# Kernel optimization log

Hardware: AMD Instinct MI355X
Metric: run time of the kernel (lower is better)

Reference implementation:

```python
import jax, jax.numpy as jnp
import numpy as np

B, R, L = 1, 256, 384
IN_DIM, PAIR_DIM, N_HEADS = 128, 128, 8
HEAD_DIM = IN_DIM // N_HEADS
FF_MULT = 4


def layer_norm(x, g, b, eps=1e-5):
    mu = jnp.mean(x, axis=-1, keepdims=True)
    var = jnp.mean((x - mu) ** 2, axis=-1, keepdims=True)
    return (x - mu) * jax.lax.rsqrt(var + eps) * g + b


def setup_inputs() -> dict:
    key = jax.random.key(0)
    ks = jax.random.split(key, 12)
    s = 0.02
    return {
        "x": jax.random.normal(ks[0], (B, L, L, PAIR_DIM), jnp.float32),
        "m": jax.random.normal(ks[1], (B, R, L, IN_DIM), jnp.float32),
        "ln1_g": jnp.ones((PAIR_DIM,), jnp.float32),
        "ln1_b": jnp.zeros((PAIR_DIM,), jnp.float32),
        "ln2_g": jnp.ones((IN_DIM,), jnp.float32),
        "ln2_b": jnp.zeros((IN_DIM,), jnp.float32),
        "ln3_g": jnp.ones((IN_DIM,), jnp.float32),
        "ln3_b": jnp.zeros((IN_DIM,), jnp.float32),
        "w1": jax.random.normal(ks[2], (PAIR_DIM, N_HEADS), jnp.float32) * s,
        "b1": jnp.zeros((N_HEADS,), jnp.float32),
        "w2": jax.random.normal(ks[3], (IN_DIM, HEAD_DIM), jnp.float32) * s,
        "b2": jnp.zeros((HEAD_DIM,), jnp.float32),
        "ffw1": jax.random.normal(ks[4], (IN_DIM, IN_DIM * FF_MULT), jnp.float32) * s,
        "ffb1": jnp.zeros((IN_DIM * FF_MULT,), jnp.float32),
        "ffw2": jax.random.normal(ks[5], (IN_DIM * FF_MULT, IN_DIM), jnp.float32) * s,
        "ffb2": jnp.zeros((IN_DIM,), jnp.float32),
    }


def reference(x, m, ln1_g, ln1_b, ln2_g, ln2_b, ln3_g, ln3_b,
              w1, b1, w2, b2, ffw1, ffb1, ffw2, ffb2):
    # symmetrize pair features: [b, i, j, d]
    pair = (x + jnp.swapaxes(x, 1, 2)) * 0.5
    pair = layer_norm(pair, ln1_g, ln1_b)
    # attention logits per head, softmax over j (axis=-2): [b, i, j, h]
    attn = jax.nn.softmax(pair @ w1 + b1, axis=-2)
    # values: [b, r, j, d_head]
    values = layer_norm(m, ln2_g, ln2_b) @ w2 + b2
    # [b,i,j,h] x [b,r,j,d] -> [b,r,i,h,d]
    attn_out = jnp.einsum('bijh,brjd->brihd', attn, values)
    attn_out = attn_out.reshape(*attn_out.shape[:3], -1)  # [b,r,i,h*d]
    out = m + attn_out
    residue = layer_norm(out, ln3_g, ln3_b)
    ff = jax.nn.relu(residue @ ffw1 + ffb1) @ ffw2 + ffb2  # dropout off (eval)
    return out + ff
```

## Files before the change

### kernel.cpp

```cpp
#include <hip/hip_runtime.h>

typedef __attribute__((ext_vector_type(8))) short bf16x8;
typedef __attribute__((ext_vector_type(4))) float f32x4;

constexpr int L  = 384;
constexpr int R  = 256;
constexpr int D  = 128;
constexpr int NH = 8;
constexpr int HD = 16;
constexpr int FF = 512;

#define MFMA16(a, b, c) __builtin_amdgcn_mfma_f32_16x16x32_bf16((a), (b), (c), 0, 0, 0)

__device__ inline unsigned short f2bf(float f) {
    unsigned u = __builtin_bit_cast(unsigned, f);
    u += 0x7fffu + ((u >> 16) & 1u);
    return (unsigned short)(u >> 16);
}
__device__ inline float bf2f(unsigned short h) {
    unsigned u = ((unsigned)h) << 16;
    return __builtin_bit_cast(float, u);
}

__device__ inline int tri_row(int q) {
    int i = (int)((769.0f - sqrtf((float)(591361 - 8 * q))) * 0.5f);
    while ((i + 1) * (769 - (i + 1)) / 2 <= q) ++i;
    while (i * (769 - i) / 2 > q) --i;
    return i;
}

__global__ void k_prep(const float* __restrict__ w1,
                       const float* __restrict__ w2,
                       const float* __restrict__ ffw1,
                       const float* __restrict__ ffw2,
                       const float* __restrict__ g3,
                       const float* __restrict__ b3,
                       const float* __restrict__ ffb1,
                       unsigned short* __restrict__ w1p,
                       unsigned short* __restrict__ w2p,
                       unsigned short* __restrict__ w1gF,
                       unsigned short* __restrict__ w2tF,
                       float2* __restrict__ c1c2) {
    const int idx = blockIdx.x * 256 + threadIdx.x;
    {
        const int fi = idx >> 9, rem = idx & 511, l = rem >> 3, e = rem & 7;
        const int lr2 = l & 15, lg2 = l >> 4;
        const int n = fi >> 2, ks = fi & 3;
        const int ch = n * 16 + lr2, k = ks * 32 + lg2 * 8 + e;
        w1gF[idx] = f2bf(g3[k] * ffw1[(size_t)k * FF + ch]);
    }
    {
        const int fi = idx >> 9, rem = idx & 511, l = rem >> 3, e = rem & 7;
        const int lr2 = l & 15, lg2 = l >> 4;
        const int n = fi >> 4, Ks = fi & 15;
        const int ch = n * 16 + lr2, k = Ks * 32 + lg2 * 8 + e;
        w2tF[idx] = f2bf(ffw2[(size_t)k * D + ch]);
    }
    if (idx < 16 * D) {
        const int n = idx >> 7, k = idx & 127;
        w1p[idx] = (n < NH) ? f2bf(w1[(size_t)k * NH + n]) : (unsigned short)0;
        w2p[idx] = f2bf(w2[(size_t)k * HD + n]);
    }
    if (blockIdx.x < 2) {
        const int n = blockIdx.x * 256 + threadIdx.x;
        float c1 = 0.f, c2 = 0.f;
        for (int k = 0; k < D; ++k) {
            const float w = ffw1[(size_t)k * FF + n];
            c1 += g3[k] * w;
            c2 += b3[k] * w;
        }
        c1c2[n] = make_float2(c1, c2 + ffb1[n]);
    }
}

__global__ void k_pair_logits(const float* __restrict__ x,
                              const float* __restrict__ g,
                              const float* __restrict__ bt,
                              const unsigned short* __restrict__ w1p,
                              const float* __restrict__ b1,
                              float* __restrict__ logits) {
    __shared__ unsigned short nrm[64][136];
    __shared__ int ij[64];
    const int tid = threadIdx.x;
    const int q0 = blockIdx.x * 64;

    {
        const int pr = tid >> 2, part = tid & 3;
        const int q = q0 + pr;
        const int i = tri_row(q);
        const int j = i + (q - i * (769 - i) / 2);
        if (part == 0) ij[pr] = (i << 16) | j;
        const float* xa = x + ((size_t)i * L + j) * D + part * 32;
        const float* xb = x + ((size_t)j * L + i) * D + part * 32;
        float v[32];
        float s = 0.f, sq = 0.f;
        #pragma unroll
        for (int q8 = 0; q8 < 8; ++q8) {
            const float4 a = ((const float4*)xa)[q8];
            const float4 b = ((const float4*)xb)[q8];
            const float t0 = 0.5f * (a.x + b.x), t1 = 0.5f * (a.y + b.y);
            const float t2 = 0.5f * (a.z + b.z), t3 = 0.5f * (a.w + b.w);
            v[q8*4+0] = t0; v[q8*4+1] = t1; v[q8*4+2] = t2; v[q8*4+3] = t3;
            s  += t0 + t1 + t2 + t3;
            sq += t0*t0 + t1*t1 + t2*t2 + t3*t3;
        }
        s  += __shfl_xor(s, 1);  s  += __shfl_xor(s, 2);
        sq += __shfl_xor(sq, 1); sq += __shfl_xor(sq, 2);
        const float mean = s * (1.0f / D);
        const float rstd = rsqrtf(sq * (1.0f / D) - mean * mean + 1e-5f);
        #pragma unroll
        for (int q8 = 0; q8 < 8; ++q8) {
            const int c = part * 32 + q8 * 4;
            ushort4 pk;
            pk.x = f2bf((v[q8*4+0] - mean) * rstd * g[c+0] + bt[c+0]);
            pk.y = f2bf((v[q8*4+1] - mean) * rstd * g[c+1] + bt[c+1]);
            pk.z = f2bf((v[q8*4+2] - mean) * rstd * g[c+2] + bt[c+2]);
            pk.w = f2bf((v[q8*4+3] - mean) * rstd * g[c+3] + bt[c+3]);
            *(ushort4*)(&nrm[pr][c]) = pk;
        }
    }
    __syncthreads();

    {
        const int wv = tid >> 6, lane = tid & 63;
        const int lr = lane & 15, lg = lane >> 4;
        f32x4 acc = {0.f, 0.f, 0.f, 0.f};
        #pragma unroll
        for (int ks = 0; ks < 4; ++ks) {
            bf16x8 a = *(const bf16x8*)(&nrm[wv * 16 + lr][ks * 32 + lg * 8]);
            bf16x8 b = *(const bf16x8*)(w1p + (size_t)lr * D + ks * 32 + lg * 8);
            acc = MFMA16(a, b, acc);
        }
        if (lr < NH) {
            #pragma unroll
            for (int r = 0; r < 4; ++r) {
                const int pl = wv * 16 + lg * 4 + r;
                const int pij = ij[pl];
                const int pi = pij >> 16, pj = pij & 0xffff;
                const float val = acc[r] + b1[lr];
                logits[((size_t)pi * L + pj) * NH + lr] = val;
                logits[((size_t)pj * L + pi) * NH + lr] = val;
            }
        }
    }
}

__global__ void k_softmax(const float* __restrict__ logits,
                          unsigned short* __restrict__ attnT) {
    const int wave = blockIdx.x * 4 + (threadIdx.x >> 6);
    const int lane = threadIdx.x & 63;
    const int i = wave >> 3, h = wave & 7;

    float v[6];
    float mx = -1e30f;
    #pragma unroll
    for (int t = 0; t < 6; ++t) {
        const int j = lane + t * 64;
        v[t] = logits[((size_t)i * L + j) * NH + h];
        mx = fmaxf(mx, v[t]);
    }
    #pragma unroll
    for (int msk = 32; msk; msk >>= 1) mx = fmaxf(mx, __shfl_xor(mx, msk));

    float s = 0.0f;
    #pragma unroll
    for (int t = 0; t < 6; ++t) { v[t] = __expf(v[t] - mx); s += v[t]; }
    #pragma unroll
    for (int msk = 32; msk; msk >>= 1) s += __shfl_xor(s, msk);
    const float inv = 1.0f / s;

    #pragma unroll
    for (int t = 0; t < 6; ++t) {
        const int j = lane + t * 64;
        attnT[((size_t)h * L + i) * L + j] = f2bf(v[t] * inv);
    }
}

__global__ void k_values(const float* __restrict__ min_,
                         const float* __restrict__ g,
                         const float* __restrict__ bt,
                         const unsigned short* __restrict__ w2p,
                         const float* __restrict__ b2,
                         unsigned short* __restrict__ VtT) {
    __shared__ unsigned short nrm[128][136];
    const int tid = threadIdx.x;
    const int r  = blockIdx.x;
    const int j0 = blockIdx.y * 128;

    #pragma unroll
    for (int half = 0; half < 2; ++half) {
        const int row  = half * 64 + (tid >> 2);
        const int part = tid & 3;
        const float* src = min_ + ((size_t)r * L + j0 + row) * D + part * 32;
        float v[32];
        float s = 0.f, sq = 0.f;
        #pragma unroll
        for (int q = 0; q < 8; ++q) {
            const float4 a = ((const float4*)src)[q];
            v[q*4+0] = a.x; v[q*4+1] = a.y; v[q*4+2] = a.z; v[q*4+3] = a.w;
            s  += a.x + a.y + a.z + a.w;
            sq += a.x*a.x + a.y*a.y + a.z*a.z + a.w*a.w;
        }
        s  += __shfl_xor(s, 1);  s  += __shfl_xor(s, 2);
        sq += __shfl_xor(sq, 1); sq += __shfl_xor(sq, 2);
        const float mean = s * (1.0f / D);
        const float rstd = rsqrtf(sq * (1.0f / D) - mean * mean + 1e-5f);
        #pragma unroll
        for (int q = 0; q < 8; ++q) {
            const int c = part * 32 + q * 4;
            ushort4 pk;
            pk.x = f2bf((v[q*4+0] - mean) * rstd * g[c+0] + bt[c+0]);
            pk.y = f2bf((v[q*4+1] - mean) * rstd * g[c+1] + bt[c+1]);
            pk.z = f2bf((v[q*4+2] - mean) * rstd * g[c+2] + bt[c+2]);
            pk.w = f2bf((v[q*4+3] - mean) * rstd * g[c+3] + bt[c+3]);
            *(ushort4*)(&nrm[row][c]) = pk;
        }
    }
    __syncthreads();

    {
        const int wv = tid >> 6, lane = tid & 63;
        const int lr = lane & 15, lg = lane >> 4;
        f32x4 acc[2];
        acc[0] = (f32x4){0.f, 0.f, 0.f, 0.f};
        acc[1] = (f32x4){0.f, 0.f, 0.f, 0.f};
        #pragma unroll
        for (int ks = 0; ks < 4; ++ks) {
            bf16x8 b = *(const bf16x8*)(w2p + (size_t)lr * D + ks * 32 + lg * 8);
            #pragma unroll
            for (int mt = 0; mt < 2; ++mt) {
                bf16x8 a = *(const bf16x8*)(&nrm[wv * 32 + mt * 16 + lr][ks * 32 + lg * 8]);
                acc[mt] = MFMA16(a, b, acc[mt]);
            }
        }
        const float bb = b2[lr];
        #pragma unroll
        for (int mt = 0; mt < 2; ++mt) {
            ushort4 pk;
            pk.x = f2bf(acc[mt][0] + bb);
            pk.y = f2bf(acc[mt][1] + bb);
            pk.z = f2bf(acc[mt][2] + bb);
            pk.w = f2bf(acc[mt][3] + bb);
            *(ushort4*)(VtT + (size_t)(r * HD + lr) * L + j0 + wv * 32 + mt * 16 + lg * 4) = pk;
        }
    }
}

__global__ void k_attn_out(const unsigned short* __restrict__ attnT,
                           const unsigned short* __restrict__ VtT,
                           const float* __restrict__ min_,
                           unsigned short* __restrict__ outb) {
    const int h  = blockIdx.z;
    const int i0 = blockIdx.x * 128;
    const int n0 = blockIdx.y * 128;
    const int tid = threadIdx.x, wv = tid >> 6, lane = tid & 63;
    const int lr = lane & 15, lg = lane >> 4;
    const int wio = (wv >> 1) * 64, wno = (wv & 1) * 64;
    const unsigned short* Abase = attnT + (size_t)h * L * L;

    f32x4 acc[4][4];
    #pragma unroll
    for (int a = 0; a < 4; ++a)
        #pragma unroll
        for (int b = 0; b < 4; ++b) acc[a][b] = (f32x4){0.f, 0.f, 0.f, 0.f};

    bf16x8 af[4], bf[4], afn[4], bfn[4];
    #pragma unroll
    for (int mt = 0; mt < 4; ++mt)
        af[mt] = *(const bf16x8*)(Abase + (size_t)(i0 + wio + mt * 16 + lr) * L + lg * 8);
    #pragma unroll
    for (int nt = 0; nt < 4; ++nt)
        bf[nt] = *(const bf16x8*)(VtT + (size_t)(n0 + wno + nt * 16 + lr) * L + lg * 8);

    for (int ks = 0; ks < 12; ++ks) {
        if (ks < 11) {
            const int ko = (ks + 1) * 32 + lg * 8;
            #pragma unroll
            for (int mt = 0; mt < 4; ++mt)
                afn[mt] = *(const bf16x8*)(Abase + (size_t)(i0 + wio + mt * 16 + lr) * L + ko);
            #pragma unroll
            for (int nt = 0; nt < 4; ++nt)
                bfn[nt] = *(const bf16x8*)(VtT + (size_t)(n0 + wno + nt * 16 + lr) * L + ko);
        }
        #pragma unroll
        for (int mt = 0; mt < 4; ++mt)
            #pragma unroll
            for (int nt = 0; nt < 4; ++nt)
                acc[mt][nt] = MFMA16(af[mt], bf[nt], acc[mt][nt]);
        #pragma unroll
        for (int q = 0; q < 4; ++q) { af[q] = afn[q]; bf[q] = bfn[q]; }
    }

    #pragma unroll
    for (int mt = 0; mt < 4; ++mt) {
        #pragma unroll
        for (int nt = 0; nt < 4; ++nt) {
            const int nbase = n0 + wno + nt * 16;
            const int rrow  = nbase >> 4;
            #pragma unroll
            for (int r = 0; r < 4; ++r) {
                const int i = i0 + wio + mt * 16 + lg * 4 + r;
                const size_t gidx = ((size_t)rrow * L + i) * D + h * HD + lr;
                outb[gidx] = f2bf(min_[gidx] + acc[mt][nt][r]);
            }
        }
    }
}

__global__ __launch_bounds__(512, 4) void k_ffn(
                      const unsigned short* __restrict__ outb,
                      const unsigned short* __restrict__ w1gF,
                      const float2* __restrict__ c1c2,
                      const unsigned short* __restrict__ w2tF,
                      const float* __restrict__ ffb2,
                      float* __restrict__ out) {
    __shared__ unsigned short At[64 * 128];
    __shared__ unsigned short hid[2][64 * 128];
    __shared__ float2 stats[64];
    const int tid = threadIdx.x;
    const size_t row0 = (size_t)blockIdx.x * 64;

    const int wv = tid >> 6, lane = tid & 63;
    const int lr = lane & 15, lg = lane >> 4;
    const int wm = wv >> 2, wn = wv & 3;

    bf16x8 w1f[8], w2f[8];
    #pragma unroll
    for (int ks = 0; ks < 4; ++ks)
        #pragma unroll
        for (int nt = 0; nt < 2; ++nt) {
            const int fi = (0 * 8 + wn * 2 + nt) * 4 + ks;
            w1f[ks * 2 + nt] = *(const bf16x8*)((const char*)w1gF + fi * 1024 + lane * 16);
        }

    {
        const int rr = tid >> 3, part = tid & 7;
        const unsigned short* src = outb + (row0 + rr) * D + part * 16;
        const uint4 v0 = *(const uint4*)(src);
        const uint4 v1 = *(const uint4*)(src + 8);
        float s = 0.f, sq = 0.f;
        const unsigned w[8] = {v0.x, v0.y, v0.z, v0.w, v1.x, v1.y, v1.z, v1.w};
        #pragma unroll
        for (int e = 0; e < 8; ++e) {
            const float lo = __builtin_bit_cast(float, w[e] << 16);
            const float hi = __builtin_bit_cast(float, w[e] & 0xffff0000u);
            s  += lo + hi;
            sq += lo * lo + hi * hi;
        }
        s  += __shfl_xor(s, 1);  s  += __shfl_xor(s, 2);  s  += __shfl_xor(s, 4);
        sq += __shfl_xor(sq, 1); sq += __shfl_xor(sq, 2); sq += __shfl_xor(sq, 4);
        if (part == 0) {
            const float mean = s * (1.0f / D);
            const float rstd = rsqrtf(sq * (1.0f / D) - mean * mean + 1e-5f);
            stats[rr] = make_float2(rstd, mean * rstd);
        }
        const int xr = (rr & 7) << 4;
        char* rowp = (char*)(At + rr * 128);
        const int cb = part * 32;
        *(uint4*)(rowp + ((cb     ) ^ xr)) = v0;
        *(uint4*)(rowp + ((cb + 16) ^ xr)) = v1;
    }

    #pragma unroll
    for (int ks = 0; ks < 4; ++ks)
        #pragma unroll
        for (int nt = 0; nt < 2; ++nt) {
            const int fi = (wn * 2 + nt) * 16 + 0 * 4 + ks;
            w2f[ks * 2 + nt] = *(const bf16x8*)((const char*)w2tF + fi * 1024 + lane * 16);
        }

    __syncthreads();

    f32x4 acc2[2][2];
    #pragma unroll
    for (int m = 0; m < 2; ++m)
        #pragma unroll
        for (int n = 0; n < 2; ++n) acc2[m][n] = (f32x4){0.f, 0.f, 0.f, 0.f};

    #pragma unroll
    for (int kc = 0; kc < 4; ++kc) {
        const int p = kc & 1;

        {
            f32x4 acc1[2][2];
            #pragma unroll
            for (int m = 0; m < 2; ++m)
                #pragma unroll
                for (int n = 0; n < 2; ++n) acc1[m][n] = (f32x4){0.f, 0.f, 0.f, 0.f};

            #pragma unroll
            for (int ks = 0; ks < 4; ++ks) {
                bf16x8 af[2];
                #pragma unroll
                for (int mt = 0; mt < 2; ++mt) {
                    const int row = wm * 32 + mt * 16 + lr;
                    af[mt] = *(const bf16x8*)((char*)(At + row * 128) +
                              ((ks * 64 + lg * 16) ^ ((row & 7) << 4)));
                }
                #pragma unroll
                for (int mt = 0; mt < 2; ++mt)
                    #pragma unroll
                    for (int nt = 0; nt < 2; ++nt)
                        acc1[mt][nt] = MFMA16(af[mt], w1f[ks * 2 + nt], acc1[mt][nt]);
            }

            #pragma unroll
            for (int nt = 0; nt < 2; ++nt) {
                const int chl = wn * 32 + nt * 16 + lr;
                const float2 cc = c1c2[kc * 128 + chl];
                #pragma unroll
                for (int mt = 0; mt < 2; ++mt) {
                    #pragma unroll
                    for (int r = 0; r < 4; ++r) {
                        const int row = wm * 32 + mt * 16 + lg * 4 + r;
                        const float2 st = stats[row];
                        const float pre = st.x * acc1[mt][nt][r] - st.y * cc.x + cc.y;
                        *(unsigned short*)((char*)(hid[p] + row * 128) +
                            ((chl * 2) ^ ((row & 7) << 4))) = f2bf(fmaxf(pre, 0.f));
                    }
                }
            }
        }
        __syncthreads();

        if (kc < 3) {
            #pragma unroll
            for (int ks = 0; ks < 4; ++ks)
                #pragma unroll
                for (int nt = 0; nt < 2; ++nt) {
                    const int fi = ((kc + 1) * 8 + wn * 2 + nt) * 4 + ks;
                    w1f[ks * 2 + nt] = *(const bf16x8*)((const char*)w1gF + fi * 1024 + lane * 16);
                }
        }

        {
            #pragma unroll
            for (int ks = 0; ks < 4; ++ks) {
                bf16x8 hf[2];
                #pragma unroll
                for (int mt = 0; mt < 2; ++mt) {
                    const int row = wm * 32 + mt * 16 + lr;
                    hf[mt] = *(const bf16x8*)((char*)(hid[p] + row * 128) +
                              ((ks * 64 + lg * 16) ^ ((row & 7) << 4)));
                }
                #pragma unroll
                for (int mt = 0; mt < 2; ++mt)
                    #pragma unroll
                    for (int nt = 0; nt < 2; ++nt)
                        acc2[mt][nt] = MFMA16(hf[mt], w2f[ks * 2 + nt], acc2[mt][nt]);
            }
        }

        if (kc < 3) {
            #pragma unroll
            for (int ks = 0; ks < 4; ++ks)
                #pragma unroll
                for (int nt = 0; nt < 2; ++nt) {
                    const int fi = (wn * 2 + nt) * 16 + (kc + 1) * 4 + ks;
                    w2f[ks * 2 + nt] = *(const bf16x8*)((const char*)w2tF + fi * 1024 + lane * 16);
                }
        }
    }

    #pragma unroll
    for (int nt = 0; nt < 2; ++nt) {
        const int ch = wn * 32 + nt * 16 + lr;
        const float bb = ffb2[ch];
        #pragma unroll
        for (int mt = 0; mt < 2; ++mt) {
            #pragma unroll
            for (int r = 0; r < 4; ++r) {
                const int row = wm * 32 + mt * 16 + lg * 4 + r;
                const float resid = bf2f(*(const unsigned short*)((char*)(At + row * 128) +
                                     ((ch * 2) ^ ((row & 7) << 4))));
                out[(row0 + row) * (size_t)D + ch] = resid + acc2[mt][nt][r] + bb;
            }
        }
    }
}

extern "C" void kernel_launch(void* const* d_in, const int* in_sizes, int n_in,
                              void* d_out, int out_size, void* d_ws, size_t ws_size,
                              hipStream_t stream) {
    const float* x     = (const float*)d_in[0];
    const float* m     = (const float*)d_in[1];
    const float* ln1_g = (const float*)d_in[2];
    const float* ln1_b = (const float*)d_in[3];
    const float* ln2_g = (const float*)d_in[4];
    const float* ln2_b = (const float*)d_in[5];
    const float* ln3_g = (const float*)d_in[6];
    const float* ln3_b = (const float*)d_in[7];
    const float* w1    = (const float*)d_in[8];
    const float* b1    = (const float*)d_in[9];
    const float* w2    = (const float*)d_in[10];
    const float* b2    = (const float*)d_in[11];
    const float* ffw1  = (const float*)d_in[12];
    const float* ffb1  = (const float*)d_in[13];
    const float* ffw2  = (const float*)d_in[14];
    const float* ffb2  = (const float*)d_in[15];

    float* out = (float*)d_out;

    char* wsp = (char*)d_ws;
    float*          logits = (float*)wsp;              wsp += (size_t)L*L*NH*4;
    unsigned short* attnT  = (unsigned short*)wsp;     wsp += (size_t)NH*L*L*2;
    unsigned short* VtT    = (unsigned short*)wsp;     wsp += (size_t)R*HD*L*2;
    unsigned short* w1gF   = (unsigned short*)wsp;     wsp += (size_t)FF*D*2;
    unsigned short* w2tF   = (unsigned short*)wsp;     wsp += (size_t)D*FF*2;
    unsigned short* w1p    = (unsigned short*)wsp;     wsp += (size_t)16*D*2;
    unsigned short* w2p    = (unsigned short*)wsp;     wsp += (size_t)16*D*2;
    float2*         c1c2   = (float2*)wsp;             wsp += (size_t)FF*8;
    unsigned short* outb   = (unsigned short*)wsp;     wsp += (size_t)R*L*D*2;

    k_prep<<<(FF * D) / 256, 256, 0, stream>>>(w1, w2, ffw1, ffw2,
                                               ln3_g, ln3_b, ffb1,
                                               w1p, w2p, w1gF, w2tF, c1c2);

    k_pair_logits<<<1155, 256, 0, stream>>>(x, ln1_g, ln1_b, w1p, b1, logits);
    k_softmax<<<(L * NH) / 4, 256, 0, stream>>>(logits, attnT);

    dim3 g3(R, L / 128);
    k_values<<<g3, 256, 0, stream>>>(m, ln2_g, ln2_b, w2p, b2, VtT);

    dim3 g4(L / 128, (R * HD) / 128, NH);
    k_attn_out<<<g4, 256, 0, stream>>>(attnT, VtT, m, outb);

    k_ffn<<<(R * L) / 64, 512, 0, stream>>>(outb, w1gF, c1c2, w2tF, ffb2, out);
}
```

Measured before the change: 147.5 us.

## Software-pipeline FFN hidden chunk computation with double-buffered hidden tile

Peels the first FFN hidden chunk (GEMM1 plus ReLU) out of the loop and, in each iteration, computes the next chunk into the alternate hidden buffer while consuming the current one in GEMM2. The single barrier moves to the end of the iteration so GEMM1 and GEMM2 MFMAs can interleave without a sync between them. This adds register pressure and relies on correct double-buffer ordering.

```diff
diff --git a/kernel.cpp b/kernel.cpp
--- a/kernel.cpp
+++ b/kernel.cpp
@@ -371,6 +371,53 @@
 
     __syncthreads();
 
+    {
+        f32x4 acc1[2][2];
+        #pragma unroll
+        for (int m = 0; m < 2; ++m)
+            #pragma unroll
+            for (int n = 0; n < 2; ++n) acc1[m][n] = (f32x4){0.f, 0.f, 0.f, 0.f};
+        #pragma unroll
+        for (int ks = 0; ks < 4; ++ks) {
+            bf16x8 af[2];
+            #pragma unroll
+            for (int mt = 0; mt < 2; ++mt) {
+                const int row = wm * 32 + mt * 16 + lr;
+                af[mt] = *(const bf16x8*)((char*)(At + row * 128) +
+                          ((ks * 64 + lg * 16) ^ ((row & 7) << 4)));
+            }
+            #pragma unroll
+            for (int mt = 0; mt < 2; ++mt)
+                #pragma unroll
+                for (int nt = 0; nt < 2; ++nt)
+                    acc1[mt][nt] = MFMA16(af[mt], w1f[ks * 2 + nt], acc1[mt][nt]);
+        }
+        #pragma unroll
+        for (int nt = 0; nt < 2; ++nt) {
+            const int chl = wn * 32 + nt * 16 + lr;
+            const float2 cc = c1c2[0 * 128 + chl];
+            #pragma unroll
+            for (int mt = 0; mt < 2; ++mt) {
+                #pragma unroll
+                for (int r = 0; r < 4; ++r) {
+                    const int row = wm * 32 + mt * 16 + lg * 4 + r;
+                    const float2 st = stats[row];
+                    const float pre = st.x * acc1[mt][nt][r] - st.y * cc.x + cc.y;
+                    *(unsigned short*)((char*)(hid[0] + row * 128) +
+                        ((chl * 2) ^ ((row & 7) << 4))) = f2bf(fmaxf(pre, 0.f));
+                }
+            }
+        }
+    }
+    #pragma unroll
+    for (int ks = 0; ks < 4; ++ks)
+        #pragma unroll
+        for (int nt = 0; nt < 2; ++nt) {
+            const int fi = (1 * 8 + wn * 2 + nt) * 4 + ks;
+            w1f[ks * 2 + nt] = *(const bf16x8*)((const char*)w1gF + fi * 1024 + lane * 16);
+        }
+    __syncthreads();
+
     f32x4 acc2[2][2];
     #pragma unroll
     for (int m = 0; m < 2; ++m)
@@ -381,13 +428,12 @@
     for (int kc = 0; kc < 4; ++kc) {
         const int p = kc & 1;
 
-        {
+        if (kc < 3) {
             f32x4 acc1[2][2];
             #pragma unroll
             for (int m = 0; m < 2; ++m)
                 #pragma unroll
                 for (int n = 0; n < 2; ++n) acc1[m][n] = (f32x4){0.f, 0.f, 0.f, 0.f};
-
             #pragma unroll
             for (int ks = 0; ks < 4; ++ks) {
                 bf16x8 af[2];
@@ -403,11 +449,10 @@
                     for (int nt = 0; nt < 2; ++nt)
                         acc1[mt][nt] = MFMA16(af[mt], w1f[ks * 2 + nt], acc1[mt][nt]);
             }
-
             #pragma unroll
             for (int nt = 0; nt < 2; ++nt) {
                 const int chl = wn * 32 + nt * 16 + lr;
-                const float2 cc = c1c2[kc * 128 + chl];
+                const float2 cc = c1c2[(kc + 1) * 128 + chl];
                 #pragma unroll
                 for (int mt = 0; mt < 2; ++mt) {
                     #pragma unroll
@@ -415,22 +460,20 @@
                         const int row = wm * 32 + mt * 16 + lg * 4 + r;
                         const float2 st = stats[row];
                         const float pre = st.x * acc1[mt][nt][r] - st.y * cc.x + cc.y;
-                        *(unsigned short*)((char*)(hid[p] + row * 128) +
+                        *(unsigned short*)((char*)(hid[p ^ 1] + row * 128) +
                             ((chl * 2) ^ ((row & 7) << 4))) = f2bf(fmaxf(pre, 0.f));
                     }
                 }
             }
-        }
-        __syncthreads();
-
-        if (kc < 3) {
-            #pragma unroll
-            for (int ks = 0; ks < 4; ++ks)
-                #pragma unroll
-                for (int nt = 0; nt < 2; ++nt) {
-                    const int fi = ((kc + 1) * 8 + wn * 2 + nt) * 4 + ks;
-                    w1f[ks * 2 + nt] = *(const bf16x8*)((const char*)w1gF + fi * 1024 + lane * 16);
-                }
+            if (kc < 2) {
+                #pragma unroll
+                for (int ks = 0; ks < 4; ++ks)
+                    #pragma unroll
+                    for (int nt = 0; nt < 2; ++nt) {
+                        const int fi = ((kc + 2) * 8 + wn * 2 + nt) * 4 + ks;
+                        w1f[ks * 2 + nt] = *(const bf16x8*)((const char*)w1gF + fi * 1024 + lane * 16);
+                    }
+            }
         }
 
         {
@@ -459,6 +502,7 @@
                     const int fi = (wn * 2 + nt) * 16 + (kc + 1) * 4 + ks;
                     w2f[ks * 2 + nt] = *(const bf16x8*)((const char*)w2tF + fi * 1024 + lane * 16);
                 }
+            __syncthreads();
         }
     }
 
```

After: 182.6 us. 23.8% more time.
